# Performance work log

Measured on AMD Instinct MI355X. Metric: run time of the kernel, lower is better.

## Reference

```python
import jax, jax.numpy as jnp
import numpy as np
import math

B, C_IN, N_SEL, N_DROP, HEADS = 4, 128, 1024, 1024, 4
Q_OUT = K_OUT = V_OUT = 256
N = N_SEL + N_DROP


def setup_inputs() -> dict:
    key = jax.random.key(0)
    ks = jax.random.split(key, 8)
    pcd_up = jax.random.normal(ks[0], (B, C_IN, N), jnp.float32)
    points_select = jax.random.normal(ks[1], (B, C_IN, N_SEL), jnp.float32)
    points_drop = jax.random.normal(ks[2], (B, C_IN, N_DROP), jnp.float32)
    # per-batch permutation of [0, N) split into select/drop halves (collision-free scatter)
    perms = jax.vmap(lambda k: jax.random.permutation(k, N))(jax.random.split(ks[3], B))
    idx_select = perms[:, None, :N_SEL].astype(jnp.int32)
    idx_drop = perms[:, None, N_SEL:].astype(jnp.int32)
    scale = 1.0 / math.sqrt(C_IN)
    Wq = jax.random.normal(ks[4], (Q_OUT, C_IN), jnp.float32) * scale
    Wk = jax.random.normal(ks[5], (K_OUT, C_IN), jnp.float32) * scale
    Wv = jax.random.normal(ks[6], (V_OUT, C_IN), jnp.float32) * scale
    Wskip = jax.random.normal(ks[7], (V_OUT, C_IN), jnp.float32) * scale
    return {"pcd_up": pcd_up, "points_select": points_select, "points_drop": points_drop,
            "idx_select": idx_select, "idx_drop": idx_drop,
            "Wq": Wq, "Wk": Wk, "Wv": Wv, "Wskip": Wskip}


def _concat_by_idx(a, b, idx_a, idx_b):
    # scatter columns of concat([a,b]) to positions given by concat([idx_a, idx_b])
    src = jnp.concatenate([a, b], axis=-1)            # (B, C, N)
    idx = jnp.concatenate([idx_a, idx_b], axis=-1)[:, 0, :]  # (B, N)
    return jax.vmap(lambda s, i: jnp.zeros_like(s).at[:, i].set(s))(src, idx)


def reference(pcd_up, points_select, points_drop, idx_select, idx_drop, Wq, Wk, Wv, Wskip):
    b, _, n = pcd_up.shape
    x = _concat_by_idx(points_select, points_drop, idx_select, idx_drop)  # (B, C_in, N)
    # 1x1 convs (no bias) == channel matmuls, then split heads: (B, H, D, N)
    q = jnp.einsum('oc,bcn->bon', Wq, x).reshape(b, HEADS, Q_OUT // HEADS, n)
    k = jnp.einsum('oc,bcn->bon', Wk, x).reshape(b, HEADS, K_OUT // HEADS, n)
    v = jnp.einsum('oc,bcn->bon', Wv, x).reshape(b, HEADS, V_OUT // HEADS, n)
    energy = jnp.einsum('bhdn,bhdm->bhnm', q, k)      # (B, H, N, N)
    attn = jax.nn.softmax(energy / math.sqrt(Q_OUT // HEADS), axis=-1)
    out = jnp.einsum('bhnm,bhdm->bhnd', attn, v)      # (B, H, N, Dv)
    out = out.transpose(0, 2, 1, 3).reshape(b, n, V_OUT).transpose(0, 2, 1)  # (B, V_out, N)
    skip = jnp.einsum('oc,bcn->bon', Wskip, pcd_up)   # (B, V_out, N)
    return skip + out
```

## Files before the change

kernel.cpp:

```cpp
#include <hip/hip_runtime.h>
#include <hip/hip_bf16.h>
#include <math.h>

#define B_    4
#define C_IN_ 128
#define N_    2048
#define NSEL_ 1024
#define H_    4
#define KS_   2

typedef __bf16 bf16;
typedef __bf16 bf16x2 __attribute__((ext_vector_type(2)));
typedef __bf16 bf16x4 __attribute__((ext_vector_type(4)));
typedef __bf16 bf16x8 __attribute__((ext_vector_type(8)));
typedef float  f32x4  __attribute__((ext_vector_type(4)));

__global__ __launch_bounds__(256) void prep_kernel(
    const int* __restrict__ isel, const int* __restrict__ idrp,
    const float* __restrict__ Wq, const float* __restrict__ Wk,
    const float* __restrict__ Wv, const float* __restrict__ Ws,
    int* __restrict__ inv, bf16* __restrict__ Wbf)
{
    const int blk = blockIdx.x;
    if (blk < 128) {
        int e = blk * 256 + threadIdx.x;
        int which = e >> 13, idx = e & 8191;
        const float* Wx = (which == 0) ? Wq : (which == 1) ? Wk
                        : (which == 2) ? Wv : Ws;
        float4 v = *(const float4*)(Wx + (size_t)idx * 4);
        bf16x4 o; o[0] = (bf16)v.x; o[1] = (bf16)v.y; o[2] = (bf16)v.z; o[3] = (bf16)v.w;
        *(bf16x4*)(Wbf + (size_t)which * 32768 + (size_t)idx * 4) = o;
    } else {
        int g = (blk - 128) * 256 + threadIdx.x;
        int b = g >> 11, j = g & (N_ - 1);
        int pos = (j < NSEL_) ? isel[b * NSEL_ + j] : idrp[b * NSEL_ + (j - NSEL_)];
        inv[b * N_ + (pos & (N_ - 1))] = j;
    }
}

#define XSTR 136

__global__ __launch_bounds__(256) void qkv_mfma_kernel(
    const float* __restrict__ pcd, const float* __restrict__ sel,
    const float* __restrict__ drop, const bf16* __restrict__ Wbf,
    bf16* __restrict__ qT, bf16* __restrict__ kTt, bf16* __restrict__ vTt,
    float* __restrict__ out)
{
    const int ntile = blockIdx.x;
    const int which = blockIdx.y >> 1;
    const int rh    = blockIdx.y & 1;
    const int b     = blockIdx.z;
    const int tid   = threadIdx.x;
    const int w     = tid >> 6;
    const int lane  = tid & 63;
    const int quad  = lane >> 4;
    const int lc    = lane & 15;
    const int n0    = ntile * 64;

    __shared__ __align__(16) bf16 xT[64 * XSTR];

    const float* srcp; int rstride;
    if (which == 3)      { srcp = pcd  + (size_t)b * C_IN_ * N_ + n0;              rstride = N_;    }
    else if (ntile < 16) { srcp = sel  + (size_t)b * C_IN_ * NSEL_ + n0;           rstride = NSEL_; }
    else                 { srcp = drop + (size_t)b * C_IN_ * NSEL_ + (n0 - NSEL_); rstride = NSEL_; }

    #pragma unroll
    for (int k = 0; k < 8; ++k) {
        int e  = tid + k * 256;
        int c  = e >> 4, nq = e & 15;
        float4 v = *(const float4*)(srcp + (size_t)c * rstride + nq * 4);
        int cc = c ^ ((nq & 3) << 3);
        xT[(nq * 4 + 0) * XSTR + cc] = (bf16)v.x;
        xT[(nq * 4 + 1) * XSTR + cc] = (bf16)v.y;
        xT[(nq * 4 + 2) * XSTR + cc] = (bf16)v.z;
        xT[(nq * 4 + 3) * XSTR + cc] = (bf16)v.w;
    }
    __syncthreads();

    const bf16* wbase = Wbf + (size_t)which * 256 * 128;
    const int rbase = rh * 128 + w * 32;

    f32x4 acc[2][4];
    #pragma unroll
    for (int mt = 0; mt < 2; ++mt)
        #pragma unroll
        for (int nt = 0; nt < 4; ++nt) acc[mt][nt] = (f32x4){0.f, 0.f, 0.f, 0.f};

    #pragma unroll
    for (int kq = 0; kq < 4; ++kq) {
        bf16x8 A[2], Bf[4];
        #pragma unroll
        for (int mt = 0; mt < 2; ++mt)
            A[mt] = *(const bf16x8*)(wbase + (size_t)(rbase + mt * 16 + lc) * 128 + kq * 32 + quad * 8);
        #pragma unroll
        for (int nt = 0; nt < 4; ++nt) {
            int row = nt * 16 + lc;
            int col = (kq * 32 + quad * 8) ^ (((row >> 2) & 3) << 3);
            Bf[nt] = *(const bf16x8*)&xT[row * XSTR + col];
        }
        #pragma unroll
        for (int mt = 0; mt < 2; ++mt)
            #pragma unroll
            for (int nt = 0; nt < 4; ++nt)
                acc[mt][nt] = __builtin_amdgcn_mfma_f32_16x16x32_bf16(A[mt], Bf[nt], acc[mt][nt], 0, 0, 0);
    }

    #pragma unroll
    for (int mt = 0; mt < 2; ++mt) {
        #pragma unroll
        for (int nt = 0; nt < 4; ++nt) {
            #pragma unroll
            for (int r = 0; r < 4; ++r) {
                int o256 = rbase + mt * 16 + quad * 4 + r;
                int n    = n0 + nt * 16 + lc;
                int rloc = nt * 16 + lc;
                float val = acc[mt][nt][r];
                if (which == 0) {
                    int h = o256 >> 6, d = o256 & 63;
                    qT[((size_t)(b * H_ + h) * N_ + n) * 64 + d] = (bf16)(val * 0.125f);
                } else if (which == 1) {
                    int h = o256 >> 6, d = o256 & 63;
                    kTt[(((size_t)(b * H_ + h) * 32 + ntile) << 12) | (rloc << 6) | d] = (bf16)val;
                } else if (which == 2) {
                    int h = o256 >> 6, dv = o256 & 63;
                    vTt[(((size_t)(b * H_ + h) * 32 + ntile) << 12) | (dv << 6) | rloc] = (bf16)val;
                } else {
                    out[((size_t)b * 256 + o256) * N_ + n] = val;
                }
            }
        }
    }
}

#define PSTR 88
#define KVSTR 72

__global__ __launch_bounds__(256) void attn_kernel(
    const bf16* __restrict__ qT, const bf16* __restrict__ kTt,
    const bf16* __restrict__ vTt, bf16* __restrict__ Opart,
    float* __restrict__ S_ws)
{
    const int id    = blockIdx.x;
    const int bh    = (id & 7) + 8 * ((id >> 3) & 1);
    const int ntile = (id >> 4) & 31;
    const int c     = id >> 9;
    const int b     = bh >> 2;
    const int h     = bh & 3;
    const int tid   = threadIdx.x;
    const int w     = tid >> 6;
    const int lane  = tid & 63;
    const int quad  = lane >> 4;
    const int lc    = lane & 15;
    const int n0    = ntile * 64;

    __shared__ __align__(16) bf16 sK[64 * KVSTR];
    __shared__ __align__(16) bf16 sV[64 * KVSTR];
    __shared__ __align__(16) bf16 p_lds[4 * 16 * PSTR];

    bf16* pw = &p_lds[w * 16 * PSTR];

    const bf16* qp = qT + ((size_t)bh * N_ + n0 + w * 16 + lc) * 64 + quad * 8;
    bf16x8 aq0 = *(const bf16x8*)(qp);
    bf16x8 aq1 = *(const bf16x8*)(qp + 32);

    const bf16* kbase = kTt + (((size_t)bh * 32 + c * 16) << 12);
    const bf16* vbase = vTt + (((size_t)bh * 32 + c * 16) << 12);

    const int l0 = (tid >> 3) * KVSTR + (tid & 7) * 8;
    const int l1 = ((tid >> 3) + 32) * KVSTR + (tid & 7) * 8;

    bf16x8 ldK0 = *(const bf16x8*)(kbase + tid * 8);
    bf16x8 ldK1 = *(const bf16x8*)(kbase + 2048 + tid * 8);
    bf16x8 ldV0 = *(const bf16x8*)(vbase + tid * 8);
    bf16x8 ldV1 = *(const bf16x8*)(vbase + 2048 + tid * 8);

    f32x4 accO[4];
    #pragma unroll
    for (int i = 0; i < 4; ++i) accO[i] = (f32x4){0.f, 0.f, 0.f, 0.f};
    float psum[4] = {0.f, 0.f, 0.f, 0.f};

    for (int s = 0; s < 16; ++s) {
        __syncthreads();
        *(bf16x8*)&sK[l0] = ldK0;
        *(bf16x8*)&sK[l1] = ldK1;
        *(bf16x8*)&sV[l0] = ldV0;
        *(bf16x8*)&sV[l1] = ldV1;
        __syncthreads();

        if (s < 15) {
            const bf16* kg = kbase + ((size_t)(s + 1) << 12);
            const bf16* vg = vbase + ((size_t)(s + 1) << 12);
            ldK0 = *(const bf16x8*)(kg + tid * 8);
            ldK1 = *(const bf16x8*)(kg + 2048 + tid * 8);
            ldV0 = *(const bf16x8*)(vg + tid * 8);
            ldV1 = *(const bf16x8*)(vg + 2048 + tid * 8);
        }

        f32x4 accS[4];
        #pragma unroll
        for (int mt = 0; mt < 4; ++mt) {
            const int rb = (mt * 16 + lc) * KVSTR + quad * 8;
            bf16x8 k0 = *(const bf16x8*)&sK[rb];
            bf16x8 k1 = *(const bf16x8*)&sK[rb + 32];
            f32x4 z = (f32x4){0.f, 0.f, 0.f, 0.f};
            z = __builtin_amdgcn_mfma_f32_16x16x32_bf16(aq0, k0, z, 0, 0, 0);
            z = __builtin_amdgcn_mfma_f32_16x16x32_bf16(aq1, k1, z, 0, 0, 0);
            accS[mt] = z;
        }

        #pragma unroll
        for (int r = 0; r < 4; ++r) {
            float sum = 0.f;
            #pragma unroll
            for (int mt = 0; mt < 4; ++mt) {
                float p = __expf(accS[mt][r]);
                accS[mt][r] = p;
                sum += p;
            }
            psum[r] += sum;
        }

        #pragma unroll
        for (int mt = 0; mt < 4; ++mt)
            #pragma unroll
            for (int r = 0; r < 4; ++r)
                pw[(quad * 4 + r) * PSTR + mt * 16 + lc] = (bf16)accS[mt][r];
        bf16x8 ap0 = *(const bf16x8*)(pw + lc * PSTR + quad * 8);
        bf16x8 ap1 = *(const bf16x8*)(pw + lc * PSTR + 32 + quad * 8);

        #pragma unroll
        for (int dvt = 0; dvt < 4; ++dvt) {
            const int rb = (dvt * 16 + lc) * KVSTR + quad * 8;
            bf16x8 v0 = *(const bf16x8*)&sV[rb];
            bf16x8 v1 = *(const bf16x8*)&sV[rb + 32];
            accO[dvt] = __builtin_amdgcn_mfma_f32_16x16x32_bf16(ap0, v0, accO[dvt], 0, 0, 0);
            accO[dvt] = __builtin_amdgcn_mfma_f32_16x16x32_bf16(ap1, v1, accO[dvt], 0, 0, 0);
        }
    }

    float inv[4];
    #pragma unroll
    for (int r = 0; r < 4; ++r) {
        float s = psum[r];
        #pragma unroll
        for (int off = 1; off < 16; off <<= 1)
            s += __shfl_xor(s, off, 64);
        inv[r] = 1.f / s;
        int n = n0 + w * 16 + quad * 4 + r;
        if (lc == 0)
            S_ws[((size_t)(c * B_ + b) * H_ + h) * N_ + n] = s;
    }

    #pragma unroll
    for (int r = 0; r < 4; ++r) {
        int n = n0 + w * 16 + quad * 4 + r;
        #pragma unroll
        for (int dvt = 0; dvt < 4; ++dvt) {
            int o = h * 64 + dvt * 16 + lc;
            Opart[((size_t)(c * B_ + b) * N_ + n) * 256 + o] = (bf16)(accO[dvt][r] * inv[r]);
        }
    }
}

__global__ __launch_bounds__(256) void scatter_kernel(
    const bf16* __restrict__ Opart, const float* __restrict__ S_ws,
    const int* __restrict__ inv, float* __restrict__ out)
{
    const int ptile = blockIdx.x;
    const int og    = blockIdx.y;
    const int b     = blockIdx.z;
    const int tid   = threadIdx.x;
    const int p0    = ptile * 64;

    __shared__ __align__(16) bf16 lds[64 * 72];
    __shared__ float wls[KS_][64];
    __shared__ int   jrow[64];

    if (tid < 64) {
        int row = tid;
        int j = inv[b * N_ + p0 + row] & (N_ - 1);
        jrow[row] = j;
        float sv[KS_]; float denom = 0.f;
        #pragma unroll
        for (int c = 0; c < KS_; ++c) {
            sv[c] = S_ws[((size_t)(c * B_ + b) * H_ + og) * N_ + j];
            denom += sv[c];
        }
        float id = 1.f / denom;
        #pragma unroll
        for (int c = 0; c < KS_; ++c) wls[c][row] = sv[c] * id;
    }
    __syncthreads();

    #pragma unroll
    for (int k = 0; k < 2; ++k) {
        int e = tid + k * 256;
        int row = e >> 3, seg = e & 7;
        int j = jrow[row];
        float a8[8];
        #pragma unroll
        for (int i = 0; i < 8; ++i) a8[i] = 0.f;
        #pragma unroll
        for (int c = 0; c < KS_; ++c) {
            bf16x8 v = *(const bf16x8*)(Opart + ((size_t)(c * B_ + b) * N_ + j) * 256 + og * 64 + seg * 8);
            float wgt = wls[c][row];
            #pragma unroll
            for (int i = 0; i < 8; ++i) a8[i] += wgt * (float)v[i];
        }
        bf16x8 o8;
        #pragma unroll
        for (int i = 0; i < 8; ++i) o8[i] = (bf16)a8[i];
        *(bf16x8*)&lds[row * 72 + seg * 8] = o8;
    }
    __syncthreads();

    const int pl  = tid & 63;
    const int og2 = tid >> 6;
    #pragma unroll
    for (int k = 0; k < 8; ++k) {
        int o_loc = og2 * 16 + k * 2;
        bf16x2 v2 = *(const bf16x2*)&lds[pl * 72 + o_loc];
        int o = og * 64 + o_loc;
        size_t a = ((size_t)b * 256 + o) * N_ + p0 + pl;
        out[a]      += (float)v2[0];
        out[a + N_] += (float)v2[1];
    }
}

extern "C" void kernel_launch(void* const* d_in, const int* in_sizes, int n_in,
                              void* d_out, int out_size, void* d_ws, size_t ws_size,
                              hipStream_t stream) {
    const float* pcd  = (const float*)d_in[0];
    const float* sel  = (const float*)d_in[1];
    const float* drop = (const float*)d_in[2];
    const int*   isel = (const int*)d_in[3];
    const int*   idrp = (const int*)d_in[4];
    const float* Wq   = (const float*)d_in[5];
    const float* Wk   = (const float*)d_in[6];
    const float* Wv   = (const float*)d_in[7];
    const float* Ws   = (const float*)d_in[8];
    float* out = (float*)d_out;

    const size_t MB = 1024 * 1024;
    char*  ws    = (char*)d_ws;
    bf16*  qT    = (bf16*)(ws);
    bf16*  kTt   = (bf16*)(ws + 4 * MB);
    bf16*  vTt   = (bf16*)(ws + 8 * MB);
    bf16*  Opart = (bf16*)(ws + 12 * MB);
    float* S_ws  = (float*)(ws + (12 + KS_ * 4) * MB);
    int*   inv   = (int*)(ws + (12 + KS_ * 4) * MB + KS_ * 128 * 1024);
    bf16*  Wbf   = Opart;

    prep_kernel<<<dim3(160), 256, 0, stream>>>(isel, idrp, Wq, Wk, Wv, Ws, inv, Wbf);
    qkv_mfma_kernel<<<dim3(32, 8, B_), 256, 0, stream>>>(pcd, sel, drop, Wbf,
                                                         qT, kTt, vTt, out);
    attn_kernel<<<dim3(32 * 16 * KS_), 256, 0, stream>>>(qT, kTt, vTt, Opart, S_ws);
    scatter_kernel<<<dim3(32, 4, B_), 256, 0, stream>>>(Opart, S_ws, inv, out);
}
```

Before: 143.2 us.

## Use single-wave attention blocks with register K/V fragments and bf16 skip buffer

The attention kernel moves from 256-thread blocks that stage K/V tiles through LDS with barriers to 64-thread blocks that each handle 16 query rows. These blocks load K and V MFMA fragments straight from global memory into registers, prefetching the next K tile. The skip projection is now written to a bf16 workspace and added in the scatter kernel, and the QKV kernel swaps MFMA operand order for q/k so stores coalesce along d. The changes remove LDS staging and syncs and halve skip write traffic, at the cost of repeated global reads of K/V per query tile and bf16 rounding of the skip term.

```diff
diff --git a/kernel.cpp b/kernel.cpp
--- a/kernel.cpp
+++ b/kernel.cpp
@@ -44,7 +44,7 @@
     const float* __restrict__ pcd, const float* __restrict__ sel,
     const float* __restrict__ drop, const bf16* __restrict__ Wbf,
     bf16* __restrict__ qT, bf16* __restrict__ kTt, bf16* __restrict__ vTt,
-    float* __restrict__ out)
+    bf16* __restrict__ skipw)
 {
     const int ntile = blockIdx.x;
     const int which = blockIdx.y >> 1;
@@ -65,114 +65,134 @@
     else                 { srcp = drop + (size_t)b * C_IN_ * NSEL_ + (n0 - NSEL_); rstride = NSEL_; }
 
     #pragma unroll
-    for (int k = 0; k < 8; ++k) {
+    for (int k = 0; k < 4; ++k) {
         int e  = tid + k * 256;
-        int c  = e >> 4, nq = e & 15;
-        float4 v = *(const float4*)(srcp + (size_t)c * rstride + nq * 4);
-        int cc = c ^ ((nq & 3) << 3);
-        xT[(nq * 4 + 0) * XSTR + cc] = (bf16)v.x;
-        xT[(nq * 4 + 1) * XSTR + cc] = (bf16)v.y;
-        xT[(nq * 4 + 2) * XSTR + cc] = (bf16)v.z;
-        xT[(nq * 4 + 3) * XSTR + cc] = (bf16)v.w;
+        int cp = e >> 4, nq = e & 15;
+        int c0 = cp * 2;
+        float4 v0 = *(const float4*)(srcp + (size_t)c0 * rstride + nq * 4);
+        float4 v1 = *(const float4*)(srcp + (size_t)(c0 + 1) * rstride + nq * 4);
+        int cc = c0 ^ ((nq & 3) << 3);
+        float a0[4] = {v0.x, v0.y, v0.z, v0.w};
+        float a1[4] = {v1.x, v1.y, v1.z, v1.w};
+        #pragma unroll
+        for (int i = 0; i < 4; ++i) {
+            int n = nq * 4 + i;
+            bf16x2 t; t[0] = (bf16)a0[i]; t[1] = (bf16)a1[i];
+            *(bf16x2*)&xT[n * XSTR + cc] = t;
+        }
     }
     __syncthreads();
 
     const bf16* wbase = Wbf + (size_t)which * 256 * 128;
     const int rbase = rh * 128 + w * 32;
 
-    f32x4 acc[2][4];
-    #pragma unroll
-    for (int mt = 0; mt < 2; ++mt)
-        #pragma unroll
-        for (int nt = 0; nt < 4; ++nt) acc[mt][nt] = (f32x4){0.f, 0.f, 0.f, 0.f};
+    f32x4 acc[8];
+    #pragma unroll
+    for (int i = 0; i < 8; ++i) acc[i] = (f32x4){0.f, 0.f, 0.f, 0.f};
 
     #pragma unroll
     for (int kq = 0; kq < 4; ++kq) {
-        bf16x8 A[2], Bf[4];
-        #pragma unroll
-        for (int mt = 0; mt < 2; ++mt)
-            A[mt] = *(const bf16x8*)(wbase + (size_t)(rbase + mt * 16 + lc) * 128 + kq * 32 + quad * 8);
+        bf16x8 wf[2], xA[4];
+        #pragma unroll
+        for (int ot = 0; ot < 2; ++ot)
+            wf[ot] = *(const bf16x8*)(wbase + (size_t)(rbase + ot * 16 + lc) * 128 + kq * 32 + quad * 8);
         #pragma unroll
         for (int nt = 0; nt < 4; ++nt) {
             int row = nt * 16 + lc;
             int col = (kq * 32 + quad * 8) ^ (((row >> 2) & 3) << 3);
-            Bf[nt] = *(const bf16x8*)&xT[row * XSTR + col];
-        }
-        #pragma unroll
-        for (int mt = 0; mt < 2; ++mt)
+            xA[nt] = *(const bf16x8*)&xT[row * XSTR + col];
+        }
+        if (which <= 1) {
             #pragma unroll
             for (int nt = 0; nt < 4; ++nt)
-                acc[mt][nt] = __builtin_amdgcn_mfma_f32_16x16x32_bf16(A[mt], Bf[nt], acc[mt][nt], 0, 0, 0);
-    }
-
-    #pragma unroll
-    for (int mt = 0; mt < 2; ++mt) {
+                #pragma unroll
+                for (int ot = 0; ot < 2; ++ot)
+                    acc[nt * 2 + ot] = __builtin_amdgcn_mfma_f32_16x16x32_bf16(xA[nt], wf[ot], acc[nt * 2 + ot], 0, 0, 0);
+        } else {
+            #pragma unroll
+            for (int ot = 0; ot < 2; ++ot)
+                #pragma unroll
+                for (int nt = 0; nt < 4; ++nt)
+                    acc[ot * 4 + nt] = __builtin_amdgcn_mfma_f32_16x16x32_bf16(wf[ot], xA[nt], acc[ot * 4 + nt], 0, 0, 0);
+        }
+    }
+
+    if (which <= 1) {
         #pragma unroll
         for (int nt = 0; nt < 4; ++nt) {
             #pragma unroll
-            for (int r = 0; r < 4; ++r) {
-                int o256 = rbase + mt * 16 + quad * 4 + r;
-                int n    = n0 + nt * 16 + lc;
-                int rloc = nt * 16 + lc;
-                float val = acc[mt][nt][r];
-                if (which == 0) {
+            for (int ot = 0; ot < 2; ++ot) {
+                #pragma unroll
+                for (int r = 0; r < 4; ++r) {
+                    int n    = n0 + nt * 16 + quad * 4 + r;
+                    int rloc = nt * 16 + quad * 4 + r;
+                    int o256 = rbase + ot * 16 + lc;
                     int h = o256 >> 6, d = o256 & 63;
-                    qT[((size_t)(b * H_ + h) * N_ + n) * 64 + d] = (bf16)(val * 0.125f);
-                } else if (which == 1) {
-                    int h = o256 >> 6, d = o256 & 63;
-                    kTt[(((size_t)(b * H_ + h) * 32 + ntile) << 12) | (rloc << 6) | d] = (bf16)val;
-                } else if (which == 2) {
-                    int h = o256 >> 6, dv = o256 & 63;
-                    vTt[(((size_t)(b * H_ + h) * 32 + ntile) << 12) | (dv << 6) | rloc] = (bf16)val;
-                } else {
-                    out[((size_t)b * 256 + o256) * N_ + n] = val;
+                    float val = acc[nt * 2 + ot][r];
+                    if (which == 0)
+                        qT[((size_t)(b * H_ + h) * N_ + n) * 64 + d] = (bf16)(val * 0.125f);
+                    else
+                        kTt[(((size_t)(b * H_ + h) * 32 + ntile) << 12) | (rloc << 6) | d] = (bf16)val;
                 }
             }
         }
-    }
-}
-
-#define PSTR 88
-#define KVSTR 72
-
-__global__ __launch_bounds__(256) void attn_kernel(
+    } else {
+        #pragma unroll
+        for (int ot = 0; ot < 2; ++ot) {
+            #pragma unroll
+            for (int nt = 0; nt < 4; ++nt) {
+                #pragma unroll
+                for (int r = 0; r < 4; ++r) {
+                    int o256 = rbase + ot * 16 + quad * 4 + r;
+                    int n    = n0 + nt * 16 + lc;
+                    int rloc = nt * 16 + lc;
+                    float val = acc[ot * 4 + nt][r];
+                    if (which == 2) {
+                        int h = o256 >> 6, dv = o256 & 63;
+                        vTt[(((size_t)(b * H_ + h) * 32 + ntile) << 12) | (dv << 6) | rloc] = (bf16)val;
+                    } else {
+                        skipw[((size_t)b * 256 + o256) * N_ + n] = (bf16)val;
+                    }
+                }
+            }
+        }
+    }
+}
+
+#define PSTR 72
+
+__global__ __launch_bounds__(64, 4) void attn_kernel(
     const bf16* __restrict__ qT, const bf16* __restrict__ kTt,
     const bf16* __restrict__ vTt, bf16* __restrict__ Opart,
     float* __restrict__ S_ws)
 {
     const int id    = blockIdx.x;
     const int bh    = (id & 7) + 8 * ((id >> 3) & 1);
-    const int ntile = (id >> 4) & 31;
-    const int c     = id >> 9;
+    const int qtile = (id >> 4) & 127;
+    const int c     = id >> 11;
     const int b     = bh >> 2;
     const int h     = bh & 3;
-    const int tid   = threadIdx.x;
-    const int w     = tid >> 6;
-    const int lane  = tid & 63;
+    const int lane  = threadIdx.x;
     const int quad  = lane >> 4;
     const int lc    = lane & 15;
-    const int n0    = ntile * 64;
-
-    __shared__ __align__(16) bf16 sK[64 * KVSTR];
-    __shared__ __align__(16) bf16 sV[64 * KVSTR];
-    __shared__ __align__(16) bf16 p_lds[4 * 16 * PSTR];
-
-    bf16* pw = &p_lds[w * 16 * PSTR];
-
-    const bf16* qp = qT + ((size_t)bh * N_ + n0 + w * 16 + lc) * 64 + quad * 8;
+    const int n0    = qtile * 16;
+
+    __shared__ __align__(16) bf16 pw[16 * PSTR];
+
+    const bf16* qp = qT + ((size_t)bh * N_ + n0 + lc) * 64 + quad * 8;
     bf16x8 aq0 = *(const bf16x8*)(qp);
     bf16x8 aq1 = *(const bf16x8*)(qp + 32);
 
     const bf16* kbase = kTt + (((size_t)bh * 32 + c * 16) << 12);
     const bf16* vbase = vTt + (((size_t)bh * 32 + c * 16) << 12);
-
-    const int l0 = (tid >> 3) * KVSTR + (tid & 7) * 8;
-    const int l1 = ((tid >> 3) + 32) * KVSTR + (tid & 7) * 8;
-
-    bf16x8 ldK0 = *(const bf16x8*)(kbase + tid * 8);
-    bf16x8 ldK1 = *(const bf16x8*)(kbase + 2048 + tid * 8);
-    bf16x8 ldV0 = *(const bf16x8*)(vbase + tid * 8);
-    bf16x8 ldV1 = *(const bf16x8*)(vbase + 2048 + tid * 8);
+    const int fo = lc * 64 + quad * 8;
+
+    bf16x8 kf[4][2];
+    #pragma unroll
+    for (int mt = 0; mt < 4; ++mt) {
+        kf[mt][0] = *(const bf16x8*)(kbase + mt * 1024 + fo);
+        kf[mt][1] = *(const bf16x8*)(kbase + mt * 1024 + fo + 32);
+    }
 
     f32x4 accO[4];
     #pragma unroll
@@ -180,32 +200,27 @@
     float psum[4] = {0.f, 0.f, 0.f, 0.f};
 
     for (int s = 0; s < 16; ++s) {
-        __syncthreads();
-        *(bf16x8*)&sK[l0] = ldK0;
-        *(bf16x8*)&sK[l1] = ldK1;
-        *(bf16x8*)&sV[l0] = ldV0;
-        *(bf16x8*)&sV[l1] = ldV1;
-        __syncthreads();
-
-        if (s < 15) {
-            const bf16* kg = kbase + ((size_t)(s + 1) << 12);
-            const bf16* vg = vbase + ((size_t)(s + 1) << 12);
-            ldK0 = *(const bf16x8*)(kg + tid * 8);
-            ldK1 = *(const bf16x8*)(kg + 2048 + tid * 8);
-            ldV0 = *(const bf16x8*)(vg + tid * 8);
-            ldV1 = *(const bf16x8*)(vg + 2048 + tid * 8);
-        }
-
         f32x4 accS[4];
         #pragma unroll
         for (int mt = 0; mt < 4; ++mt) {
-            const int rb = (mt * 16 + lc) * KVSTR + quad * 8;
-            bf16x8 k0 = *(const bf16x8*)&sK[rb];
-            bf16x8 k1 = *(const bf16x8*)&sK[rb + 32];
             f32x4 z = (f32x4){0.f, 0.f, 0.f, 0.f};
-            z = __builtin_amdgcn_mfma_f32_16x16x32_bf16(aq0, k0, z, 0, 0, 0);
-            z = __builtin_amdgcn_mfma_f32_16x16x32_bf16(aq1, k1, z, 0, 0, 0);
+            z = __builtin_amdgcn_mfma_f32_16x16x32_bf16(aq0, kf[mt][0], z, 0, 0, 0);
+            z = __builtin_amdgcn_mfma_f32_16x16x32_bf16(aq1, kf[mt][1], z, 0, 0, 0);
             accS[mt] = z;
+        }
+
+        bf16x8 vf[4][2];
+        const bf16* vg = vbase + ((size_t)s << 12);
+        #pragma unroll
+        for (int dvt = 0; dvt < 4; ++dvt) {
+            vf[dvt][0] = *(const bf16x8*)(vg + dvt * 1024 + fo);
+            vf[dvt][1] = *(const bf16x8*)(vg + dvt * 1024 + fo + 32);
+        }
+        const bf16* kg = kbase + ((size_t)((s + 1) & 15) << 12);
+        #pragma unroll
+        for (int mt = 0; mt < 4; ++mt) {
+            kf[mt][0] = *(const bf16x8*)(kg + mt * 1024 + fo);
+            kf[mt][1] = *(const bf16x8*)(kg + mt * 1024 + fo + 32);
         }
 
         #pragma unroll
@@ -225,16 +240,13 @@
             #pragma unroll
             for (int r = 0; r < 4; ++r)
                 pw[(quad * 4 + r) * PSTR + mt * 16 + lc] = (bf16)accS[mt][r];
-        bf16x8 ap0 = *(const bf16x8*)(pw + lc * PSTR + quad * 8);
-        bf16x8 ap1 = *(const bf16x8*)(pw + lc * PSTR + 32 + quad * 8);
+        bf16x8 ap0 = *(const bf16x8*)(&pw[lc * PSTR + quad * 8]);
+        bf16x8 ap1 = *(const bf16x8*)(&pw[lc * PSTR + 32 + quad * 8]);
 
         #pragma unroll
         for (int dvt = 0; dvt < 4; ++dvt) {
-            const int rb = (dvt * 16 + lc) * KVSTR + quad * 8;
-            bf16x8 v0 = *(const bf16x8*)&sV[rb];
-            bf16x8 v1 = *(const bf16x8*)&sV[rb + 32];
-            accO[dvt] = __builtin_amdgcn_mfma_f32_16x16x32_bf16(ap0, v0, accO[dvt], 0, 0, 0);
-            accO[dvt] = __builtin_amdgcn_mfma_f32_16x16x32_bf16(ap1, v1, accO[dvt], 0, 0, 0);
+            accO[dvt] = __builtin_amdgcn_mfma_f32_16x16x32_bf16(ap0, vf[dvt][0], accO[dvt], 0, 0, 0);
+            accO[dvt] = __builtin_amdgcn_mfma_f32_16x16x32_bf16(ap1, vf[dvt][1], accO[dvt], 0, 0, 0);
         }
     }
 
@@ -246,14 +258,14 @@
         for (int off = 1; off < 16; off <<= 1)
             s += __shfl_xor(s, off, 64);
         inv[r] = 1.f / s;
-        int n = n0 + w * 16 + quad * 4 + r;
+        int n = n0 + quad * 4 + r;
         if (lc == 0)
             S_ws[((size_t)(c * B_ + b) * H_ + h) * N_ + n] = s;
     }
 
     #pragma unroll
     for (int r = 0; r < 4; ++r) {
-        int n = n0 + w * 16 + quad * 4 + r;
+        int n = n0 + quad * 4 + r;
         #pragma unroll
         for (int dvt = 0; dvt < 4; ++dvt) {
             int o = h * 64 + dvt * 16 + lc;
@@ -264,7 +276,8 @@
 
 __global__ __launch_bounds__(256) void scatter_kernel(
     const bf16* __restrict__ Opart, const float* __restrict__ S_ws,
-    const int* __restrict__ inv, float* __restrict__ out)
+    const int* __restrict__ inv, const bf16* __restrict__ skipw,
+    float* __restrict__ out)
 {
     const int ptile = blockIdx.x;
     const int og    = blockIdx.y;
@@ -322,8 +335,10 @@
         bf16x2 v2 = *(const bf16x2*)&lds[pl * 72 + o_loc];
         int o = og * 64 + o_loc;
         size_t a = ((size_t)b * 256 + o) * N_ + p0 + pl;
-        out[a]      += (float)v2[0];
-        out[a + N_] += (float)v2[1];
+        float s0 = (float)skipw[a];
+        float s1 = (float)skipw[a + N_];
+        out[a]      = s0 + (float)v2[0];
+        out[a + N_] = s1 + (float)v2[1];
     }
 }
 
@@ -347,13 +362,14 @@
     bf16*  kTt   = (bf16*)(ws + 4 * MB);
     bf16*  vTt   = (bf16*)(ws + 8 * MB);
     bf16*  Opart = (bf16*)(ws + 12 * MB);
-    float* S_ws  = (float*)(ws + (12 + KS_ * 4) * MB);
-    int*   inv   = (int*)(ws + (12 + KS_ * 4) * MB + KS_ * 128 * 1024);
+    bf16*  skipw = (bf16*)(ws + 20 * MB);
+    float* S_ws  = (float*)(ws + 24 * MB + 512 * 1024);
+    int*   inv   = (int*)(ws + 24 * MB + 512 * 1024 + 256 * 1024);
     bf16*  Wbf   = Opart;
 
     prep_kernel<<<dim3(160), 256, 0, stream>>>(isel, idrp, Wq, Wk, Wv, Ws, inv, Wbf);
     qkv_mfma_kernel<<<dim3(32, 8, B_), 256, 0, stream>>>(pcd, sel, drop, Wbf,
-                                                         qT, kTt, vTt, out);
-    attn_kernel<<<dim3(32 * 16 * KS_), 256, 0, stream>>>(qT, kTt, vTt, Opart, S_ws);
-    scatter_kernel<<<dim3(32, 4, B_), 256, 0, stream>>>(Opart, S_ws, inv, out);
-}
+                                                         qT, kTt, vTt, skipw);
+    attn_kernel<<<dim3(128 * 16 * KS_), 64, 0, stream>>>(qT, kTt, vTt, Opart, S_ws);
+    scatter_kernel<<<dim3(32, 4, B_), 256, 0, stream>>>(Opart, S_ws, inv, skipw, out);
+}
```

Result: slower. 209.8 us (+46.4%).
